# Performance work log

Measured on AMD Instinct MI355X. Metric: run time of the kernel, lower is better.

Reference implementation:

```python
import jax, jax.numpy as jnp
import numpy as np
from jax import lax

B, T, H = 32768, 64, 16
VOCAB_USER = 600001
VOCAB_LAUNCH = 3


def setup_inputs() -> dict:
    key = jax.random.key(0)
    ks = jax.random.split(key, 10)
    s = 1.0 / np.sqrt(H)
    return {
        "user_id": jax.random.randint(ks[0], (B,), 0, VOCAB_USER),
        "launch_seq": jax.random.randint(ks[1], (B, T), 0, VOCAB_LAUNCH),
        "user_emb": jax.random.normal(ks[2], (VOCAB_USER, H), dtype=jnp.float32),
        "launch_emb": jax.random.normal(ks[3], (VOCAB_LAUNCH, H), dtype=jnp.float32),
        "W_ih": jax.random.uniform(ks[4], (3 * H, H), jnp.float32, -s, s),
        "W_hh": jax.random.uniform(ks[5], (3 * H, H), jnp.float32, -s, s),
        "b_ih": jax.random.uniform(ks[6], (3 * H,), jnp.float32, -s, s),
        "b_hh": jax.random.uniform(ks[7], (3 * H,), jnp.float32, -s, s),
        "fc_W": jax.random.uniform(ks[8], (1, 2 * H), jnp.float32, -s, s),
        "fc_b": jax.random.uniform(ks[9], (1,), jnp.float32, -s, s),
    }


def reference(user_id, launch_seq, user_emb, launch_emb, W_ih, W_hh, b_ih, b_hh, fc_W, fc_b):
    u = user_emb[user_id]                      # (B, H)
    x = launch_emb[launch_seq]                 # (B, T, H)
    # precompute input contributions to the gates for all timesteps
    gx_all = jnp.einsum('bth,gh->btg', x, W_ih) + b_ih  # (B, T, 3H)

    def step(h, gx):
        gh = h @ W_hh.T + b_hh                 # (B, 3H)
        r = jax.nn.sigmoid(gx[:, :H] + gh[:, :H])
        z = jax.nn.sigmoid(gx[:, H:2 * H] + gh[:, H:2 * H])
        n = jnp.tanh(gx[:, 2 * H:] + r * gh[:, 2 * H:])
        h_new = (1.0 - z) * n + z * h
        return h_new, h_new

    h0 = jnp.zeros((x.shape[0], H), dtype=x.dtype)
    _, hs = lax.scan(step, h0, jnp.swapaxes(gx_all, 0, 1))  # hs: (T, B, H)
    pooled = jnp.mean(hs, axis=0)              # (B, H)
    fc_in = jnp.concatenate([u, pooled], axis=1)  # (B, 2H)
    return fc_in @ fc_W.T + fc_b               # (B, 1)
```

## Files before the change

### kernel.cpp

```cpp
#include <hip/hip_runtime.h>
#include <hip/hip_bf16.h>
#include <string.h>


#define NBLK 2048

typedef __attribute__((ext_vector_type(8))) short    short8;
typedef __attribute__((ext_vector_type(4))) float    floatx4;
typedef __attribute__((ext_vector_type(4))) unsigned uintx4;

static __device__ __forceinline__ float fexp2(float x) { return __builtin_amdgcn_exp2f(x); }
static __device__ __forceinline__ float frcp(float x)  { return __builtin_amdgcn_rcpf(x); }
static __device__ __forceinline__ unsigned f2u(float f) { unsigned u; memcpy(&u, &f, 4); return u; }
static __device__ __forceinline__ float u2f(unsigned u) { float f; memcpy(&f, &u, 4); return f; }
static __device__ __forceinline__ float sel3(int c, float a0, float a1, float a2) {
    return c == 0 ? a0 : (c == 1 ? a1 : a2);
}

__global__ __launch_bounds__(64) void gru_mfma(
    const int* __restrict__ user_id,
    const int* __restrict__ launch_seq,
    const float* __restrict__ user_emb,
    const float* __restrict__ launch_emb,
    const float* __restrict__ W_ih,
    const float* __restrict__ W_hh,
    const float* __restrict__ b_ih,
    const float* __restrict__ b_hh,
    const float* __restrict__ fc_W,
    const float* __restrict__ fc_b,
    float* __restrict__ out)
{
    constexpr float L  = 1.4426950408889634f;
    constexpr float L2 = 2.8853900817779268f;

    __shared__ float         gxlut[144];
    __shared__ unsigned char seqT[1024];

    const int tid  = threadIdx.x;
    const int col  = tid & 15;
    const int quad = tid >> 4;
    const long long sampBase = (long long)blockIdx.x * 16;

    {
        int r = tid >> 2, w = tid & 3;
        const int* sp = launch_seq + (sampBase + r) * 64 + w * 16;
        #pragma unroll
        for (int g = 0; g < 4; ++g) {
            int4 v = ((const int4*)sp)[g];
            int t0 = w * 16 + g * 4;
            seqT[(t0 + 0) * 16 + r] = (unsigned char)v.x;
            seqT[(t0 + 1) * 16 + r] = (unsigned char)v.y;
            seqT[(t0 + 2) * 16 + r] = (unsigned char)v.z;
            seqT[(t0 + 3) * 16 + r] = (unsigned char)v.w;
        }
    }

    for (int idx = tid; idx < 144; idx += 64) {
        int s = idx / 48, g = idx - s * 48;
        float dot = b_ih[g];
        #pragma unroll
        for (int k = 0; k < 16; ++k)
            dot = fmaf(W_ih[g * 16 + k], launch_emb[s * 16 + k], dot);
        int gate = g >> 4, dim = g & 15;
        gxlut[(gate * 3 + s) * 16 + dim] =
            (g < 32) ? (-L * (dot + b_hh[g])) : (L2 * dot);
    }

    short8 Wrh, Wrl, Wzh, Wzl, Wnh, Wnl;
    {
        auto makeW = [&](int goff, float scale, short8& Hi, short8& Lo) {
            float w[8];
            if (quad < 2) {
                const float* row = W_hh + (goff + col) * 16 + quad * 8;
                float4 a = *(const float4*)row;
                float4 b = *(const float4*)(row + 4);
                w[0] = scale * a.x; w[1] = scale * a.y; w[2] = scale * a.z; w[3] = scale * a.w;
                w[4] = scale * b.x; w[5] = scale * b.y; w[6] = scale * b.z; w[7] = scale * b.w;
            } else {
                #pragma unroll
                for (int j = 0; j < 8; ++j) w[j] = 0.f;
            }
            uintx4 hi, lo;
            #pragma unroll
            for (int p = 0; p < 4; ++p) {
                unsigned u0 = f2u(w[2 * p]), u1 = f2u(w[2 * p + 1]);
                hi[p] = __builtin_amdgcn_perm(u1, u0, 0x07060302u);
                float l0 = w[2 * p]     - u2f(u0 & 0xffff0000u);
                float l1 = w[2 * p + 1] - u2f(u1 & 0xffff0000u);
                lo[p] = __builtin_amdgcn_perm(f2u(l1), f2u(l0), 0x07060302u);
            }
            Hi = __builtin_bit_cast(short8, hi);
            Lo = __builtin_bit_cast(short8, lo);
        };
        makeW(0,  -L, Wrh, Wrl);
        makeW(16, -L, Wzh, Wzl);
        makeW(32,  L2, Wnh, Wnl);
    }

    floatx4 CnInit;
    {
        float4 bh = *(const float4*)&b_hh[32 + quad * 4];
        CnInit = floatx4{L2 * bh.x, L2 * bh.y, L2 * bh.z, L2 * bh.w};
    }

    __syncthreads();

    floatx4 gr0 = *(const floatx4*)&gxlut[(0 * 3 + 0) * 16 + quad * 4];
    floatx4 gr1 = *(const floatx4*)&gxlut[(0 * 3 + 1) * 16 + quad * 4];
    floatx4 gr2 = *(const floatx4*)&gxlut[(0 * 3 + 2) * 16 + quad * 4];
    floatx4 gz0 = *(const floatx4*)&gxlut[(1 * 3 + 0) * 16 + quad * 4];
    floatx4 gz1 = *(const floatx4*)&gxlut[(1 * 3 + 1) * 16 + quad * 4];
    floatx4 gz2 = *(const floatx4*)&gxlut[(1 * 3 + 2) * 16 + quad * 4];
    floatx4 gn0 = *(const floatx4*)&gxlut[(2 * 3 + 0) * 16 + quad * 4];
    floatx4 gn1 = *(const floatx4*)&gxlut[(2 * 3 + 1) * 16 + quad * 4];
    floatx4 gn2 = *(const floatx4*)&gxlut[(2 * 3 + 2) * 16 + quad * 4];

    const int a1 = (col + 32 * (quad & 1)) * 4;
    const int a2 = a1 + 64;

    floatx4 h    = {0.f, 0.f, 0.f, 0.f};
    floatx4 pool = {0.f, 0.f, 0.f, 0.f};
    short8 Bhi = {0, 0, 0, 0, 0, 0, 0, 0};
    short8 Blo = {0, 0, 0, 0, 0, 0, 0, 0};
    int c = seqT[col];

    #pragma unroll 4
    for (int t = 0; t < 64; ++t) {
        floatx4 accr, accz, gnv;
        #pragma unroll
        for (int i = 0; i < 4; ++i) {
            accr[i] = sel3(c, gr0[i], gr1[i], gr2[i]);
            accz[i] = sel3(c, gz0[i], gz1[i], gz2[i]);
            gnv[i]  = sel3(c, gn0[i], gn1[i], gn2[i]);
        }
        int cn = seqT[((t + 1) & 63) * 16 + col];

        accr = __builtin_amdgcn_mfma_f32_16x16x32_bf16(Wrh, Bhi, accr, 0, 0, 0);
        accz = __builtin_amdgcn_mfma_f32_16x16x32_bf16(Wzh, Bhi, accz, 0, 0, 0);
        floatx4 accn = __builtin_amdgcn_mfma_f32_16x16x32_bf16(Wnh, Bhi, CnInit, 0, 0, 0);
        accr = __builtin_amdgcn_mfma_f32_16x16x32_bf16(Wrl, Bhi, accr, 0, 0, 0);
        accz = __builtin_amdgcn_mfma_f32_16x16x32_bf16(Wzl, Bhi, accz, 0, 0, 0);
        accn = __builtin_amdgcn_mfma_f32_16x16x32_bf16(Wnl, Bhi, accn, 0, 0, 0);
        accr = __builtin_amdgcn_mfma_f32_16x16x32_bf16(Wrh, Blo, accr, 0, 0, 0);
        accz = __builtin_amdgcn_mfma_f32_16x16x32_bf16(Wzh, Blo, accz, 0, 0, 0);
        accn = __builtin_amdgcn_mfma_f32_16x16x32_bf16(Wnh, Blo, accn, 0, 0, 0);

        #pragma unroll
        for (int i = 0; i < 4; ++i) {
            float r  = frcp(1.0f + fexp2(accr[i]));
            float z  = frcp(1.0f + fexp2(accz[i]));
            float y  = fmaf(r, accn[i], gnv[i]);
            float n  = fmaf(-2.0f, frcp(1.0f + fexp2(y)), 1.0f);
            float hn = fmaf(z, h[i] - n, n);
            h[i] = hn;
            pool[i] += hn;
        }

        unsigned u0 = f2u(h[0]), u1 = f2u(h[1]), u2 = f2u(h[2]), u3 = f2u(h[3]);
        unsigned hp0 = __builtin_amdgcn_perm(u1, u0, 0x07060302u);
        unsigned hp1 = __builtin_amdgcn_perm(u3, u2, 0x07060302u);
        float l0 = h[0] - u2f(u0 & 0xffff0000u);
        float l1 = h[1] - u2f(u1 & 0xffff0000u);
        float l2 = h[2] - u2f(u2 & 0xffff0000u);
        float l3 = h[3] - u2f(u3 & 0xffff0000u);
        unsigned lp0 = __builtin_amdgcn_perm(f2u(l1), f2u(l0), 0x07060302u);
        unsigned lp1 = __builtin_amdgcn_perm(f2u(l3), f2u(l2), 0x07060302u);

        uintx4 bh4, bl4;
        bh4[0] = (unsigned)__builtin_amdgcn_ds_bpermute(a1, (int)hp0);
        bh4[1] = (unsigned)__builtin_amdgcn_ds_bpermute(a1, (int)hp1);
        bh4[2] = (unsigned)__builtin_amdgcn_ds_bpermute(a2, (int)hp0);
        bh4[3] = (unsigned)__builtin_amdgcn_ds_bpermute(a2, (int)hp1);
        bl4[0] = (unsigned)__builtin_amdgcn_ds_bpermute(a1, (int)lp0);
        bl4[1] = (unsigned)__builtin_amdgcn_ds_bpermute(a1, (int)lp1);
        bl4[2] = (unsigned)__builtin_amdgcn_ds_bpermute(a2, (int)lp0);
        bl4[3] = (unsigned)__builtin_amdgcn_ds_bpermute(a2, (int)lp1);
        Bhi = __builtin_bit_cast(short8, bh4);
        Blo = __builtin_bit_cast(short8, bl4);
        c = cn;
    }

    float4 fc1 = *(const float4*)&fc_W[quad * 4];
    float4 fc2 = *(const float4*)&fc_W[16 + quad * 4];
    int uid = user_id[sampBase + col];
    float4 u4 = *(const float4*)&user_emb[(long long)uid * 16 + quad * 4];
    const float inv64 = 1.0f / 64.0f;
    float val = fc1.x * u4.x + fc1.y * u4.y + fc1.z * u4.z + fc1.w * u4.w;
    val = fmaf(fc2.x * inv64, pool[0], val);
    val = fmaf(fc2.y * inv64, pool[1], val);
    val = fmaf(fc2.z * inv64, pool[2], val);
    val = fmaf(fc2.w * inv64, pool[3], val);
    val += __shfl_xor(val, 16);
    val += __shfl_xor(val, 32);
    if (quad == 0) out[sampBase + col] = val + fc_b[0];
}

extern "C" void kernel_launch(void* const* d_in, const int* in_sizes, int n_in,
                              void* d_out, int out_size, void* d_ws, size_t ws_size,
                              hipStream_t stream) {
    const int*   user_id    = (const int*)d_in[0];
    const int*   launch_seq = (const int*)d_in[1];
    const float* user_emb   = (const float*)d_in[2];
    const float* launch_emb = (const float*)d_in[3];
    const float* W_ih       = (const float*)d_in[4];
    const float* W_hh       = (const float*)d_in[5];
    const float* b_ih       = (const float*)d_in[6];
    const float* b_hh       = (const float*)d_in[7];
    const float* fc_W       = (const float*)d_in[8];
    const float* fc_b       = (const float*)d_in[9];
    float* out = (float*)d_out;

    gru_mfma<<<dim3(NBLK), dim3(64), 0, stream>>>(
        user_id, launch_seq, user_emb, launch_emb,
        W_ih, W_hh, b_ih, b_hh, fc_W, fc_b, out);
}
```

Baseline: 138.1 us.

## Fold input-gate lookup into MFMA one-hot rows and interleave two GRU chains

Each wave now processes 32 samples as two independent recurrent chains (L and R), interleaved so one chain's MFMA latency overlaps the other's transcendental math, and the grid is halved. The per-step input-gate lookup for r/z and the n-gate hidden bias are folded into unused K rows of the weight matrix and paired with a one-hot/constant column in the B operand, which removes the selects and accumulator initialisation. The hidden state is now sent as a single rounded bf16 value instead of a hi/lo split, dropping three MFMAs and four bpermutes per step. The trade-off is lower precision in the recurrent state and fewer, heavier blocks, which may reduce occupancy.

```diff
diff --git a/kernel.cpp b/kernel.cpp
--- a/kernel.cpp
+++ b/kernel.cpp
@@ -3,7 +3,7 @@
 #include <string.h>
 
 
-#define NBLK 2048
+#define NBLK 1024
 
 typedef __attribute__((ext_vector_type(8))) short    short8;
 typedef __attribute__((ext_vector_type(4))) float    floatx4;
@@ -11,8 +11,15 @@
 
 static __device__ __forceinline__ float fexp2(float x) { return __builtin_amdgcn_exp2f(x); }
 static __device__ __forceinline__ float frcp(float x)  { return __builtin_amdgcn_rcpf(x); }
-static __device__ __forceinline__ unsigned f2u(float f) { unsigned u; memcpy(&u, &f, 4); return u; }
-static __device__ __forceinline__ float u2f(unsigned u) { float f; memcpy(&f, &u, 4); return f; }
+static __device__ __forceinline__ unsigned short bfrne(float f) {
+    union { __hip_bfloat16 b; unsigned short u; } cv; cv.b = __float2bfloat16(f); return cv.u;
+}
+static __device__ __forceinline__ float bf2f(unsigned short u) {
+    unsigned v = ((unsigned)u) << 16; float f; memcpy(&f, &v, 4); return f;
+}
+static __device__ __forceinline__ unsigned pkbf(float a, float b) {
+    return (unsigned)bfrne(a) | ((unsigned)bfrne(b) << 16);
+}
 static __device__ __forceinline__ float sel3(int c, float a0, float a1, float a2) {
     return c == 0 ? a0 : (c == 1 ? a1 : a2);
 }
@@ -34,24 +41,25 @@
     constexpr float L2 = 2.8853900817779268f;
 
     __shared__ float         gxlut[144];
-    __shared__ unsigned char seqT[1024];
+    __shared__ unsigned char seqT[2048];
 
     const int tid  = threadIdx.x;
     const int col  = tid & 15;
     const int quad = tid >> 4;
-    const long long sampBase = (long long)blockIdx.x * 16;
+    const bool isq2 = (quad == 2);
+    const long long sampBase = (long long)blockIdx.x * 32;
 
     {
-        int r = tid >> 2, w = tid & 3;
-        const int* sp = launch_seq + (sampBase + r) * 64 + w * 16;
+        int r = tid >> 1, w = tid & 1;
+        const int* sp = launch_seq + (sampBase + r) * 64 + w * 32;
         #pragma unroll
-        for (int g = 0; g < 4; ++g) {
+        for (int g = 0; g < 8; ++g) {
             int4 v = ((const int4*)sp)[g];
-            int t0 = w * 16 + g * 4;
-            seqT[(t0 + 0) * 16 + r] = (unsigned char)v.x;
-            seqT[(t0 + 1) * 16 + r] = (unsigned char)v.y;
-            seqT[(t0 + 2) * 16 + r] = (unsigned char)v.z;
-            seqT[(t0 + 3) * 16 + r] = (unsigned char)v.w;
+            int t0 = w * 32 + g * 4;
+            seqT[(t0 + 0) * 32 + r] = (unsigned char)v.x;
+            seqT[(t0 + 1) * 32 + r] = (unsigned char)v.y;
+            seqT[(t0 + 2) * 32 + r] = (unsigned char)v.z;
+            seqT[(t0 + 3) * 32 + r] = (unsigned char)v.w;
         }
     }
 
@@ -66,133 +74,124 @@
             (g < 32) ? (-L * (dot + b_hh[g])) : (L2 * dot);
     }
 
+    __syncthreads();
+
     short8 Wrh, Wrl, Wzh, Wzl, Wnh, Wnl;
     {
-        auto makeW = [&](int goff, float scale, short8& Hi, short8& Lo) {
+        auto makeW = [&](int goff, float scale, const float* gx3, float extra19,
+                         short8& Hi, short8& Lo) {
             float w[8];
+            #pragma unroll
+            for (int j = 0; j < 8; ++j) w[j] = 0.f;
             if (quad < 2) {
                 const float* row = W_hh + (goff + col) * 16 + quad * 8;
-                float4 a = *(const float4*)row;
-                float4 b = *(const float4*)(row + 4);
-                w[0] = scale * a.x; w[1] = scale * a.y; w[2] = scale * a.z; w[3] = scale * a.w;
-                w[4] = scale * b.x; w[5] = scale * b.y; w[6] = scale * b.z; w[7] = scale * b.w;
-            } else {
                 #pragma unroll
-                for (int j = 0; j < 8; ++j) w[j] = 0.f;
+                for (int j = 0; j < 8; ++j) w[j] = scale * row[j];
+            } else if (quad == 2) {
+                if (gx3) { w[0] = gx3[col]; w[1] = gx3[16 + col]; w[2] = gx3[32 + col]; }
+                w[3] = extra19;
             }
             uintx4 hi, lo;
             #pragma unroll
             for (int p = 0; p < 4; ++p) {
-                unsigned u0 = f2u(w[2 * p]), u1 = f2u(w[2 * p + 1]);
-                hi[p] = __builtin_amdgcn_perm(u1, u0, 0x07060302u);
-                float l0 = w[2 * p]     - u2f(u0 & 0xffff0000u);
-                float l1 = w[2 * p + 1] - u2f(u1 & 0xffff0000u);
-                lo[p] = __builtin_amdgcn_perm(f2u(l1), f2u(l0), 0x07060302u);
+                unsigned short h0 = bfrne(w[2 * p]), h1 = bfrne(w[2 * p + 1]);
+                hi[p] = (unsigned)h0 | ((unsigned)h1 << 16);
+                lo[p] = pkbf(w[2 * p] - bf2f(h0), w[2 * p + 1] - bf2f(h1));
             }
             Hi = __builtin_bit_cast(short8, hi);
             Lo = __builtin_bit_cast(short8, lo);
         };
-        makeW(0,  -L, Wrh, Wrl);
-        makeW(16, -L, Wzh, Wzl);
-        makeW(32,  L2, Wnh, Wnl);
-    }
-
-    floatx4 CnInit;
-    {
-        float4 bh = *(const float4*)&b_hh[32 + quad * 4];
-        CnInit = floatx4{L2 * bh.x, L2 * bh.y, L2 * bh.z, L2 * bh.w};
-    }
-
-    __syncthreads();
-
-    floatx4 gr0 = *(const floatx4*)&gxlut[(0 * 3 + 0) * 16 + quad * 4];
-    floatx4 gr1 = *(const floatx4*)&gxlut[(0 * 3 + 1) * 16 + quad * 4];
-    floatx4 gr2 = *(const floatx4*)&gxlut[(0 * 3 + 2) * 16 + quad * 4];
-    floatx4 gz0 = *(const floatx4*)&gxlut[(1 * 3 + 0) * 16 + quad * 4];
-    floatx4 gz1 = *(const floatx4*)&gxlut[(1 * 3 + 1) * 16 + quad * 4];
-    floatx4 gz2 = *(const floatx4*)&gxlut[(1 * 3 + 2) * 16 + quad * 4];
-    floatx4 gn0 = *(const floatx4*)&gxlut[(2 * 3 + 0) * 16 + quad * 4];
-    floatx4 gn1 = *(const floatx4*)&gxlut[(2 * 3 + 1) * 16 + quad * 4];
-    floatx4 gn2 = *(const floatx4*)&gxlut[(2 * 3 + 2) * 16 + quad * 4];
+        makeW(0,  -L, &gxlut[0],  0.f,                  Wrh, Wrl);
+        makeW(16, -L, &gxlut[48], 0.f,                  Wzh, Wzl);
+        makeW(32,  L2, (const float*)0, L2 * b_hh[32 + col], Wnh, Wnl);
+    }
+
+    floatx4 gn0 = *(const floatx4*)&gxlut[(6 + 0) * 16 + quad * 4];
+    floatx4 gn1 = *(const floatx4*)&gxlut[(6 + 1) * 16 + quad * 4];
+    floatx4 gn2 = *(const floatx4*)&gxlut[(6 + 2) * 16 + quad * 4];
 
     const int a1 = (col + 32 * (quad & 1)) * 4;
     const int a2 = a1 + 64;
 
-    floatx4 h    = {0.f, 0.f, 0.f, 0.f};
-    floatx4 pool = {0.f, 0.f, 0.f, 0.f};
-    short8 Bhi = {0, 0, 0, 0, 0, 0, 0, 0};
-    short8 Blo = {0, 0, 0, 0, 0, 0, 0, 0};
-    int c = seqT[col];
-
-    #pragma unroll 4
-    for (int t = 0; t < 64; ++t) {
-        floatx4 accr, accz, gnv;
+    floatx4 hL = {0,0,0,0}, poolL = {0,0,0,0};
+    floatx4 hR = {0,0,0,0}, poolR = {0,0,0,0};
+    int cL = seqT[col];
+    int cR = seqT[16 + col];
+    short8 BL, BR;
+    {
+        unsigned P0 = (cL == 0 ? 0x3F80u : 0u) | (cL == 1 ? 0x3F800000u : 0u);
+        unsigned P1 = (cL == 2 ? 0x3F80u : 0u) | 0x3F800000u;
+        uintx4 b = {isq2 ? P0 : 0u, isq2 ? P1 : 0u, 0u, 0u};
+        BL = __builtin_bit_cast(short8, b);
+        P0 = (cR == 0 ? 0x3F80u : 0u) | (cR == 1 ? 0x3F800000u : 0u);
+        P1 = (cR == 2 ? 0x3F80u : 0u) | 0x3F800000u;
+        uintx4 b2 = {isq2 ? P0 : 0u, isq2 ? P1 : 0u, 0u, 0u};
+        BR = __builtin_bit_cast(short8, b2);
+    }
+
+    const floatx4 CZ = {0.f, 0.f, 0.f, 0.f};
+
+    auto step = [&](floatx4& h, floatx4& pool, short8& B, int& c, int base, int t) {
+        floatx4 accr = __builtin_amdgcn_mfma_f32_16x16x32_bf16(Wrh, B, CZ, 0, 0, 0);
+        floatx4 accz = __builtin_amdgcn_mfma_f32_16x16x32_bf16(Wzh, B, CZ, 0, 0, 0);
+        floatx4 accn = __builtin_amdgcn_mfma_f32_16x16x32_bf16(Wnh, B, CZ, 0, 0, 0);
+        accr = __builtin_amdgcn_mfma_f32_16x16x32_bf16(Wrl, B, accr, 0, 0, 0);
+        accz = __builtin_amdgcn_mfma_f32_16x16x32_bf16(Wzl, B, accz, 0, 0, 0);
+        accn = __builtin_amdgcn_mfma_f32_16x16x32_bf16(Wnl, B, accn, 0, 0, 0);
+
+        int cn = seqT[((t + 1) & 63) * 32 + base + col];
+
         #pragma unroll
         for (int i = 0; i < 4; ++i) {
-            accr[i] = sel3(c, gr0[i], gr1[i], gr2[i]);
-            accz[i] = sel3(c, gz0[i], gz1[i], gz2[i]);
-            gnv[i]  = sel3(c, gn0[i], gn1[i], gn2[i]);
-        }
-        int cn = seqT[((t + 1) & 63) * 16 + col];
-
-        accr = __builtin_amdgcn_mfma_f32_16x16x32_bf16(Wrh, Bhi, accr, 0, 0, 0);
-        accz = __builtin_amdgcn_mfma_f32_16x16x32_bf16(Wzh, Bhi, accz, 0, 0, 0);
-        floatx4 accn = __builtin_amdgcn_mfma_f32_16x16x32_bf16(Wnh, Bhi, CnInit, 0, 0, 0);
-        accr = __builtin_amdgcn_mfma_f32_16x16x32_bf16(Wrl, Bhi, accr, 0, 0, 0);
-        accz = __builtin_amdgcn_mfma_f32_16x16x32_bf16(Wzl, Bhi, accz, 0, 0, 0);
-        accn = __builtin_amdgcn_mfma_f32_16x16x32_bf16(Wnl, Bhi, accn, 0, 0, 0);
-        accr = __builtin_amdgcn_mfma_f32_16x16x32_bf16(Wrh, Blo, accr, 0, 0, 0);
-        accz = __builtin_amdgcn_mfma_f32_16x16x32_bf16(Wzh, Blo, accz, 0, 0, 0);
-        accn = __builtin_amdgcn_mfma_f32_16x16x32_bf16(Wnh, Blo, accn, 0, 0, 0);
-
-        #pragma unroll
-        for (int i = 0; i < 4; ++i) {
+            float gnv = sel3(c, gn0[i], gn1[i], gn2[i]);
             float r  = frcp(1.0f + fexp2(accr[i]));
             float z  = frcp(1.0f + fexp2(accz[i]));
-            float y  = fmaf(r, accn[i], gnv[i]);
+            float y  = fmaf(r, accn[i], gnv);
             float n  = fmaf(-2.0f, frcp(1.0f + fexp2(y)), 1.0f);
             float hn = fmaf(z, h[i] - n, n);
             h[i] = hn;
             pool[i] += hn;
         }
 
-        unsigned u0 = f2u(h[0]), u1 = f2u(h[1]), u2 = f2u(h[2]), u3 = f2u(h[3]);
-        unsigned hp0 = __builtin_amdgcn_perm(u1, u0, 0x07060302u);
-        unsigned hp1 = __builtin_amdgcn_perm(u3, u2, 0x07060302u);
-        float l0 = h[0] - u2f(u0 & 0xffff0000u);
-        float l1 = h[1] - u2f(u1 & 0xffff0000u);
-        float l2 = h[2] - u2f(u2 & 0xffff0000u);
-        float l3 = h[3] - u2f(u3 & 0xffff0000u);
-        unsigned lp0 = __builtin_amdgcn_perm(f2u(l1), f2u(l0), 0x07060302u);
-        unsigned lp1 = __builtin_amdgcn_perm(f2u(l3), f2u(l2), 0x07060302u);
-
-        uintx4 bh4, bl4;
-        bh4[0] = (unsigned)__builtin_amdgcn_ds_bpermute(a1, (int)hp0);
-        bh4[1] = (unsigned)__builtin_amdgcn_ds_bpermute(a1, (int)hp1);
-        bh4[2] = (unsigned)__builtin_amdgcn_ds_bpermute(a2, (int)hp0);
-        bh4[3] = (unsigned)__builtin_amdgcn_ds_bpermute(a2, (int)hp1);
-        bl4[0] = (unsigned)__builtin_amdgcn_ds_bpermute(a1, (int)lp0);
-        bl4[1] = (unsigned)__builtin_amdgcn_ds_bpermute(a1, (int)lp1);
-        bl4[2] = (unsigned)__builtin_amdgcn_ds_bpermute(a2, (int)lp0);
-        bl4[3] = (unsigned)__builtin_amdgcn_ds_bpermute(a2, (int)lp1);
-        Bhi = __builtin_bit_cast(short8, bh4);
-        Blo = __builtin_bit_cast(short8, bl4);
+        unsigned hp0 = pkbf(h[0], h[1]);
+        unsigned hp1 = pkbf(h[2], h[3]);
+        unsigned P0 = (cn == 0 ? 0x3F80u : 0u) | (cn == 1 ? 0x3F800000u : 0u);
+        unsigned P1 = (cn == 2 ? 0x3F80u : 0u) | 0x3F800000u;
+        uintx4 b;
+        b[0] = (unsigned)__builtin_amdgcn_ds_bpermute(a1, (int)hp0);
+        b[1] = (unsigned)__builtin_amdgcn_ds_bpermute(a1, (int)hp1);
+        b[2] = (unsigned)__builtin_amdgcn_ds_bpermute(a2, (int)hp0);
+        b[3] = (unsigned)__builtin_amdgcn_ds_bpermute(a2, (int)hp1);
+        b[0] = isq2 ? P0 : b[0];
+        b[1] = isq2 ? P1 : b[1];
+        B = __builtin_bit_cast(short8, b);
         c = cn;
+    };
+
+    #pragma unroll 2
+    for (int t = 0; t < 64; ++t) {
+        step(hL, poolL, BL, cL, 0, t);
+        step(hR, poolR, BR, cR, 16, t);
     }
 
     float4 fc1 = *(const float4*)&fc_W[quad * 4];
     float4 fc2 = *(const float4*)&fc_W[16 + quad * 4];
-    int uid = user_id[sampBase + col];
-    float4 u4 = *(const float4*)&user_emb[(long long)uid * 16 + quad * 4];
     const float inv64 = 1.0f / 64.0f;
-    float val = fc1.x * u4.x + fc1.y * u4.y + fc1.z * u4.z + fc1.w * u4.w;
-    val = fmaf(fc2.x * inv64, pool[0], val);
-    val = fmaf(fc2.y * inv64, pool[1], val);
-    val = fmaf(fc2.z * inv64, pool[2], val);
-    val = fmaf(fc2.w * inv64, pool[3], val);
-    val += __shfl_xor(val, 16);
-    val += __shfl_xor(val, 32);
-    if (quad == 0) out[sampBase + col] = val + fc_b[0];
+    #pragma unroll
+    for (int chain = 0; chain < 2; ++chain) {
+        const floatx4& pool = chain ? poolR : poolL;
+        long long s = sampBase + chain * 16 + col;
+        int uid = user_id[s];
+        float4 u4 = *(const float4*)&user_emb[(long long)uid * 16 + quad * 4];
+        float val = fc1.x * u4.x + fc1.y * u4.y + fc1.z * u4.z + fc1.w * u4.w;
+        val = fmaf(fc2.x * inv64, pool[0], val);
+        val = fmaf(fc2.y * inv64, pool[1], val);
+        val = fmaf(fc2.z * inv64, pool[2], val);
+        val = fmaf(fc2.w * inv64, pool[3], val);
+        val += __shfl_xor(val, 16);
+        val += __shfl_xor(val, 32);
+        if (quad == 0) out[s] = val + fc_b[0];
+    }
 }
 
 extern "C" void kernel_launch(void* const* d_in, const int* in_sizes, int n_in,
```

Measured after the change: 133.7 us. 1.03x faster.
